# Kernel tuning notes

Measured on AMD Instinct MI355X. Metric: run time of the kernel, lower is better.

## Reference

```python
import jax, jax.numpy as jnp
import numpy as np


def setup_inputs() -> dict:
    key = jax.random.key(0)
    ks = jax.random.split(key, 5)
    b, f, h, w, c = 2, 16, 64, 64, 256
    heads, D = 8, 32
    hD = heads * D
    x = jax.random.normal(ks[0], (b, f, h, w, c), dtype=jnp.float32)
    s = 1.0 / np.sqrt(c)
    Wq = jax.random.normal(ks[1], (c, hD), dtype=jnp.float32) * s
    Wk = jax.random.normal(ks[2], (c, hD), dtype=jnp.float32) * s
    Wv = jax.random.normal(ks[3], (c, hD), dtype=jnp.float32) * s
    Wo = jax.random.normal(ks[4], (hD, c), dtype=jnp.float32) * s
    return {"x": x, "Wq": Wq, "Wk": Wk, "Wv": Wv, "Wo": Wo, "heads": heads}


def reference(x, Wq, Wk, Wv, Wo, heads):
    b, f, h, w, c = x.shape
    hD = Wq.shape[1]
    D = hD // heads
    n = h * w
    # fuse batch & frames; 1x1 conv == channel matmul
    xf = x.reshape(b * f, n, c)  # [(bf), n, c]

    def proj(W):
        # [(bf), n, hD] -> [(bf), heads, D, n]
        p = jnp.einsum('bnc,cd->bnd', xf, W)
        return p.reshape(b * f, n, heads, D).transpose(0, 2, 3, 1)

    q = jax.nn.softmax(proj(Wq), axis=-2)  # softmax over D (note: scale is dead code in source)
    k = jax.nn.softmax(proj(Wk), axis=-1)  # softmax over spatial n
    v = proj(Wv)
    context = jnp.einsum('bhdn,bhen->bhde', k, v)      # [(bf), heads, D, D]
    out = jnp.einsum('bhde,bhdn->bhen', context, q)    # [(bf), heads, D, n]
    out = out.transpose(0, 3, 1, 2).reshape(b * f, n, hD)
    out = jnp.einsum('bnd,dc->bnc', out, Wo)
    return out.reshape(b, f, h, w, c)
```

## Files before the change

### kernel.cpp

```cpp
#include <hip/hip_runtime.h>
#include <hip/hip_bf16.h>


typedef __attribute__((ext_vector_type(8))) short bf16x8;
typedef __attribute__((ext_vector_type(4))) float f32x4;

__device__ __forceinline__ unsigned short f2bf(float x) {
  __hip_bfloat16 h = __float2bfloat16(x);
  union { __hip_bfloat16 b; unsigned short u; } c; c.b = h; return c.u;
}

__device__ __forceinline__ void bar_lds() {
  asm volatile("s_waitcnt lgkmcnt(0)" ::: "memory");
  __builtin_amdgcn_s_barrier();
}

__global__ __launch_bounds__(256) void k0_prep(const float* __restrict__ Wq,
                                               const float* __restrict__ Wk,
                                               const float* __restrict__ Wv,
                                               unsigned short* __restrict__ WqT,
                                               unsigned short* __restrict__ WkvT) {
  int r = blockIdx.x, c = threadIdx.x;
  if (r < 256)      WqT [(r      )*256 + c] = f2bf(Wq[c*256 + r]);
  else if (r < 512) WkvT[(r - 256)*256 + c] = f2bf(Wk[c*256 + (r-256)]);
  else              WkvT[(r - 256)*256 + c] = f2bf(Wv[c*256 + (r-512)]);
}

__global__ __launch_bounds__(1024, 4) void k1w(const float* __restrict__ x,
                                               const unsigned short* __restrict__ WkvT,
                                               float* __restrict__ ctxp) {
  __shared__ unsigned short As[2][32*256];
  __shared__ unsigned short slab[2][512*40];
  int bid = blockIdx.x;
  size_t rowbase = (size_t)bid * 512;
  int tid = threadIdx.x;
  int lane = tid & 63, w = tid >> 6;
  int cl = lane & 15, rq = (lane >> 4) << 2, fs = lane >> 4;
  int h = w & 7;
  bool isV = w >= 8;

  bf16x8 bfr[2][8];
#pragma unroll
  for (int ni = 0; ni < 2; ++ni)
#pragma unroll
    for (int kk = 0; kk < 8; ++kk)
      bfr[ni][kk] = *(const bf16x8*)(WkvT + (size_t)(w*32 + ni*16 + cl)*256 + kk*32 + fs*8);
#pragma unroll
  for (int ni = 0; ni < 2; ++ni)
#pragma unroll
    for (int kk = 0; kk < 8; ++kk)
      asm volatile("" : "+v"(bfr[ni][kk]));

  f32x4 c2[2] = {};
  float dena0 = 0.f, dena1 = 0.f;

  int ar = tid >> 5, as_ = tid & 31;
  int aw = ar*256 + ((as_ ^ (ar & 7)) << 3);
  const float* ap = x + (rowbase + ar)*256 + as_*8;

  int ca0 = h*32 + cl, ca1 = h*32 + 16 + cl;
  int cb  = 256 + h*32 + (isV ? 16 : 0) + cl;
  int ra0 = ca0*40 + fs*8;
  int ra1 = ca1*40 + fs*8;
  int rb  = cb*40  + fs*8;

  f32x4 acc[2][2];

  auto stageA = [&](int buf, float4 v0, float4 v1) {
    unsigned short* Ab = &As[buf][0];
    union { ushort4 u4[2]; int4 i4; } pk;
    pk.u4[0].x = f2bf(v0.x); pk.u4[0].y = f2bf(v0.y); pk.u4[0].z = f2bf(v0.z); pk.u4[0].w = f2bf(v0.w);
    pk.u4[1].x = f2bf(v1.x); pk.u4[1].y = f2bf(v1.y); pk.u4[1].z = f2bf(v1.z); pk.u4[1].w = f2bf(v1.w);
    *(int4*)(&Ab[aw]) = pk.i4;
  };
  auto mainMFMA = [&](int buf) {
    unsigned short* Ab = &As[buf][0];
#pragma unroll
    for (int m = 0; m < 2; ++m)
#pragma unroll
      for (int ni = 0; ni < 2; ++ni) acc[m][ni] = (f32x4){};
#pragma unroll
    for (int kk = 0; kk < 8; ++kk) {
      int so = (((kk*4 + fs) ^ (cl & 7)) << 3);
      bf16x8 a0 = *(const bf16x8*)(&Ab[cl*256 + so]);
      bf16x8 a1 = *(const bf16x8*)(&Ab[(16 + cl)*256 + so]);
#pragma unroll
      for (int ni = 0; ni < 2; ++ni) {
        acc[0][ni] = __builtin_amdgcn_mfma_f32_16x16x32_bf16(a0, bfr[ni][kk], acc[0][ni], 0, 0, 0);
        acc[1][ni] = __builtin_amdgcn_mfma_f32_16x16x32_bf16(a1, bfr[ni][kk], acc[1][ni], 0, 0, 0);
      }
    }
  };
  auto slabWrite = [&](int buf) {
    unsigned short* sb = &slab[buf][0];
#pragma unroll
    for (int ni = 0; ni < 2; ++ni) {
      int c = w*32 + ni*16 + cl;
#pragma unroll
      for (int m = 0; m < 2; ++m) {
        int n4 = m*16 + rq;
        ushort4 wv;
        if (!isV) {
          float e0 = __expf(acc[m][ni][0]), e1 = __expf(acc[m][ni][1]);
          float e2 = __expf(acc[m][ni][2]), e3 = __expf(acc[m][ni][3]);
          if (ni == 0) dena0 += (e0 + e1) + (e2 + e3); else dena1 += (e0 + e1) + (e2 + e3);
          wv.x = f2bf(e0); wv.y = f2bf(e1); wv.z = f2bf(e2); wv.w = f2bf(e3);
        } else {
          wv.x = f2bf(acc[m][ni][0]); wv.y = f2bf(acc[m][ni][1]);
          wv.z = f2bf(acc[m][ni][2]); wv.w = f2bf(acc[m][ni][3]);
        }
        *(ushort4*)(&sb[c*40 + n4]) = wv;
      }
    }
  };
  auto ctxMFMA = [&](int buf) {
    unsigned short* sb = &slab[buf][0];
    bf16x8 af0 = *(const bf16x8*)(&sb[ra0]);
    bf16x8 af1 = *(const bf16x8*)(&sb[ra1]);
    bf16x8 bv  = *(const bf16x8*)(&sb[rb]);
    c2[0] = __builtin_amdgcn_mfma_f32_16x16x32_bf16(af0, bv, c2[0], 0, 0, 0);
    c2[1] = __builtin_amdgcn_mfma_f32_16x16x32_bf16(af1, bv, c2[1], 0, 0, 0);
  };

  float4 pa0 = *(const float4*)ap;
  float4 pa1 = *(const float4*)(ap + 4);
  stageA(0, pa0, pa1);
  {
    const float* apn = ap + 32*256;
    pa0 = *(const float4*)apn;
    pa1 = *(const float4*)(apn + 4);
  }
  bar_lds();
  mainMFMA(0);

  for (int t = 0; t < 15; ++t) {
    slabWrite(t & 1);
    stageA((t + 1) & 1, pa0, pa1);
    bar_lds();
    if (t < 14) {
      const float* apn = ap + (size_t)(t + 2)*32*256;
      pa0 = *(const float4*)apn;
      pa1 = *(const float4*)(apn + 4);
    }
    ctxMFMA(t & 1);
    mainMFMA((t + 1) & 1);
  }
  slabWrite(1);
  bar_lds();
  ctxMFMA(1);

  float* cp = ctxp + ((size_t)bid*8 + h)*1056;
  int ec = isV ? 16 + cl : cl;
#pragma unroll
  for (int di = 0; di < 2; ++di)
#pragma unroll
    for (int r = 0; r < 4; ++r)
      cp[(di*16 + rq + r)*33 + ec] = c2[di][r];
  if (!isV) {
    dena0 += __shfl_xor(dena0, 16); dena0 += __shfl_xor(dena0, 32);
    dena1 += __shfl_xor(dena1, 16); dena1 += __shfl_xor(dena1, 32);
    if (fs == 0) {
      cp[cl*33 + 32]        = dena0;
      cp[(16 + cl)*33 + 32] = dena1;
    }
  }
}

__global__ __launch_bounds__(256) void k2b_w2(const float* __restrict__ ctxp,
                                              const float* __restrict__ Wo,
                                              unsigned short* __restrict__ W2t) {
  __shared__ float clds[32*33];
  int bid = blockIdx.x;
  int h = bid & 7, bfi = bid >> 3;
  int tid = threadIdx.x;
  for (int i = tid; i < 1056; i += 256) {
    float s = 0.f;
#pragma unroll
    for (int p = 0; p < 8; ++p)
      s += ctxp[((size_t)(bfi*8 + p)*8 + h)*1056 + i];
    clds[i] = s;
  }
  __syncthreads();
  float acc[32] = {};
#pragma unroll 4
  for (int e = 0; e < 32; ++e) {
    float w = Wo[(size_t)(h*32 + e)*256 + tid];
#pragma unroll
    for (int d = 0; d < 32; ++d) acc[d] += clds[d*33 + e] * w;
  }
  unsigned short* o = W2t + ((size_t)bfi*256 + tid)*256 + h*32;
#pragma unroll
  for (int d = 0; d < 32; ++d) o[d] = f2bf(acc[d] / clds[d*33 + 32]);
}

__global__ __launch_bounds__(512, 2) void k3s(const float* __restrict__ x,
                                              const unsigned short* __restrict__ WqT,
                                              const unsigned short* __restrict__ W2t,
                                              float* __restrict__ out) {
  __shared__ unsigned short As[2][32*256];
  __shared__ unsigned short Qs[2][32*256];
  int bid = blockIdx.x;
  size_t rowbase = (size_t)bid * 256;
  int bfi = bid >> 4;
  int tid = threadIdx.x;
  int lane = tid & 63, wid = tid >> 6;
  int cl = lane & 15, rq = (lane >> 4) << 2, fs = lane >> 4;

  bf16x8 bq[2][8], bw[2][8];
#pragma unroll
  for (int nf = 0; nf < 2; ++nf)
#pragma unroll
    for (int kk = 0; kk < 8; ++kk) {
      bq[nf][kk] = *(const bf16x8*)(WqT + (size_t)(wid*32 + nf*16 + cl)*256 + kk*32 + fs*8);
      bw[nf][kk] = *(const bf16x8*)(W2t + ((size_t)bfi*256 + wid*32 + nf*16 + cl)*256 + kk*32 + fs*8);
    }

  int ar = tid >> 5, as_ = tid & 31;
  int aw0 = ar*256 + ((as_ ^ (ar & 7)) << 3);
  int aw1 = (16 + ar)*256 + ((as_ ^ (ar & 7)) << 3);
  const float* ap = x + (rowbase + ar)*256 + as_*8;

  int qslotbase = wid*4 + (rq >> 3);
  ushort4 qpk[2][2];

  auto stageA = [&](int buf, float4 v0, float4 v1, float4 v2, float4 v3) {
    unsigned short* Ab = &As[buf][0];
    union { ushort4 u4[2]; int4 i4; } pk;
    pk.u4[0].x = f2bf(v0.x); pk.u4[0].y = f2bf(v0.y); pk.u4[0].z = f2bf(v0.z); pk.u4[0].w = f2bf(v0.w);
    pk.u4[1].x = f2bf(v1.x); pk.u4[1].y = f2bf(v1.y); pk.u4[1].z = f2bf(v1.z); pk.u4[1].w = f2bf(v1.w);
    *(int4*)(&Ab[aw0]) = pk.i4;
    pk.u4[0].x = f2bf(v2.x); pk.u4[0].y = f2bf(v2.y); pk.u4[0].z = f2bf(v2.z); pk.u4[0].w = f2bf(v2.w);
    pk.u4[1].x = f2bf(v3.x); pk.u4[1].y = f2bf(v3.y); pk.u4[1].z = f2bf(v3.z); pk.u4[1].w = f2bf(v3.w);
    *(int4*)(&Ab[aw1]) = pk.i4;
  };
  auto p1soft = [&](int buf) {
    unsigned short* Ab = &As[buf][0];
    f32x4 ql[2][2] = {};
#pragma unroll
    for (int kk = 0; kk < 8; ++kk) {
      int so = (((kk*4 + fs) ^ (cl & 7)) << 3);
      bf16x8 a0 = *(const bf16x8*)(&Ab[cl*256 + so]);
      bf16x8 a1 = *(const bf16x8*)(&Ab[(16 + cl)*256 + so]);
#pragma unroll
      for (int nf = 0; nf < 2; ++nf) {
        ql[0][nf] = __builtin_amdgcn_mfma_f32_16x16x32_bf16(bq[nf][kk], a0, ql[0][nf], 0, 0, 0);
        ql[1][nf] = __builtin_amdgcn_mfma_f32_16x16x32_bf16(bq[nf][kk], a1, ql[1][nf], 0, 0, 0);
      }
    }
#pragma unroll
    for (int m = 0; m < 2; ++m) {
      float e0[4], e1[4]; float s8 = 0.f;
#pragma unroll
      for (int r = 0; r < 4; ++r) { e0[r] = __expf(ql[m][0][r]); e1[r] = __expf(ql[m][1][r]); s8 += e0[r] + e1[r]; }
      float s = s8; s += __shfl_xor(s, 16); s += __shfl_xor(s, 32);
      float inv = 1.0f / s;
      qpk[m][0].x = f2bf(e0[0]*inv); qpk[m][0].y = f2bf(e0[1]*inv); qpk[m][0].z = f2bf(e0[2]*inv); qpk[m][0].w = f2bf(e0[3]*inv);
      qpk[m][1].x = f2bf(e1[0]*inv); qpk[m][1].y = f2bf(e1[1]*inv); qpk[m][1].z = f2bf(e1[2]*inv); qpk[m][1].w = f2bf(e1[3]*inv);
    }
  };
  auto qwrite = [&](int buf) {
    unsigned short* Qb = &Qs[buf][0];
#pragma unroll
    for (int m = 0; m < 2; ++m) {
      int row = m*16 + cl;
#pragma unroll
      for (int nf = 0; nf < 2; ++nf) {
        int slot = qslotbase + nf*2;
        *(ushort4*)(&Qb[row*256 + ((slot ^ (row & 7)) << 3) + (rq & 4)]) = qpk[m][nf];
      }
    }
  };

  float4 pa0 = *(const float4*)ap;
  float4 pa1 = *(const float4*)(ap + 4);
  float4 pa2 = *(const float4*)(ap + 16*256);
  float4 pa3 = *(const float4*)(ap + 16*256 + 4);
  stageA(0, pa0, pa1, pa2, pa3);
  {
    const float* apn = ap + 32*256;
    pa0 = *(const float4*)apn;
    pa1 = *(const float4*)(apn + 4);
    pa2 = *(const float4*)(apn + 16*256);
    pa3 = *(const float4*)(apn + 16*256 + 4);
  }
  bar_lds();
  p1soft(0);

  for (int t = 0; t < 7; ++t) {
    stageA((t + 1) & 1, pa0, pa1, pa2, pa3);
    qwrite(t & 1);
    bar_lds();
    if (t < 6) {
      const float* apn = ap + (size_t)(t + 2)*32*256;
      pa0 = *(const float4*)apn;
      pa1 = *(const float4*)(apn + 4);
      pa2 = *(const float4*)(apn + 16*256);
      pa3 = *(const float4*)(apn + 16*256 + 4);
    }
    f32x4 oa[2][2] = {};
    {
      unsigned short* Qb = &Qs[t & 1][0];
#pragma unroll
      for (int kk = 0; kk < 8; ++kk) {
        int so = (((kk*4 + fs) ^ (cl & 7)) << 3);
        bf16x8 q0 = *(const bf16x8*)(&Qb[cl*256 + so]);
        bf16x8 q1 = *(const bf16x8*)(&Qb[(16 + cl)*256 + so]);
#pragma unroll
        for (int nf = 0; nf < 2; ++nf) {
          oa[0][nf] = __builtin_amdgcn_mfma_f32_16x16x32_bf16(bw[nf][kk], q0, oa[0][nf], 0, 0, 0);
          oa[1][nf] = __builtin_amdgcn_mfma_f32_16x16x32_bf16(bw[nf][kk], q1, oa[1][nf], 0, 0, 0);
        }
      }
    }
    p1soft((t + 1) & 1);
#pragma unroll
    for (int m = 0; m < 2; ++m)
#pragma unroll
      for (int nf = 0; nf < 2; ++nf)
        *(f32x4*)(&out[(rowbase + (size_t)t*32 + m*16 + cl)*256 + wid*32 + nf*16 + rq]) = oa[m][nf];
  }
  qwrite(1);
  bar_lds();
  {
    unsigned short* Qb = &Qs[1][0];
    f32x4 oa[2][2] = {};
#pragma unroll
    for (int kk = 0; kk < 8; ++kk) {
      int so = (((kk*4 + fs) ^ (cl & 7)) << 3);
      bf16x8 q0 = *(const bf16x8*)(&Qb[cl*256 + so]);
      bf16x8 q1 = *(const bf16x8*)(&Qb[(16 + cl)*256 + so]);
#pragma unroll
      for (int nf = 0; nf < 2; ++nf) {
        oa[0][nf] = __builtin_amdgcn_mfma_f32_16x16x32_bf16(bw[nf][kk], q0, oa[0][nf], 0, 0, 0);
        oa[1][nf] = __builtin_amdgcn_mfma_f32_16x16x32_bf16(bw[nf][kk], q1, oa[1][nf], 0, 0, 0);
      }
    }
#pragma unroll
    for (int m = 0; m < 2; ++m)
#pragma unroll
      for (int nf = 0; nf < 2; ++nf)
        *(f32x4*)(&out[(rowbase + (size_t)7*32 + m*16 + cl)*256 + wid*32 + nf*16 + rq]) = oa[m][nf];
  }
}

extern "C" void kernel_launch(void* const* d_in, const int* in_sizes, int n_in,
                              void* d_out, int out_size, void* d_ws, size_t ws_size,
                              hipStream_t stream) {
  const float* x  = (const float*)d_in[0];
  const float* Wq = (const float*)d_in[1];
  const float* Wk = (const float*)d_in[2];
  const float* Wv = (const float*)d_in[3];
  const float* Wo = (const float*)d_in[4];
  float* out = (float*)d_out;

  unsigned short* WkvT = (unsigned short*)d_ws;
  unsigned short* WqT  = WkvT + 131072;
  unsigned short* W2t  = WqT  + 65536;
  float*          ctxp = (float*)(W2t + 2097152);

  k0_prep <<<768,  256,  0, stream>>>(Wq, Wk, Wv, WqT, WkvT);
  k1w     <<<256,  1024, 0, stream>>>(x, WkvT, ctxp);
  k2b_w2  <<<256,  256,  0, stream>>>(ctxp, Wo, W2t);
  k3s     <<<512,  512,  0, stream>>>(x, WqT, W2t, out);
}
```

Before: 131.5 us.

## Compute Q softmax in the K/V pass and stream bf16 Q to the output kernel

The Q projection and its softmax over D move from the final kernel into the first pass over x, which already stages x tiles in LDS. Each wave runs extra MFMAs against WqT and combines partial sums with a neighbouring wave through a small LDS buffer. The normalized Q is written to a global bf16 workspace. The last kernel then reads that bf16 Q instead of re-reading fp32 x and redoing the projection. This removes a second fp32 read of x and duplicate projection work. In exchange it adds a bf16 Q round trip through memory, more register pressure in the 1024-thread kernel (the register pinning asm is dropped), and per-kk global loads of WqT inside the main loop.

After: 277.6 us. +111.2%, slower.

```diff
diff --git a/kernel.cpp b/kernel.cpp
--- a/kernel.cpp
+++ b/kernel.cpp
@@ -26,11 +26,14 @@
   else              WkvT[(r - 256)*256 + c] = f2bf(Wv[c*256 + (r-512)]);
 }
 
-__global__ __launch_bounds__(1024, 4) void k1w(const float* __restrict__ x,
+__global__ __launch_bounds__(1024, 4) void k1q(const float* __restrict__ x,
                                                const unsigned short* __restrict__ WkvT,
-                                               float* __restrict__ ctxp) {
+                                               const unsigned short* __restrict__ WqT,
+                                               float* __restrict__ ctxp,
+                                               unsigned short* __restrict__ Qs) {
   __shared__ unsigned short As[2][32*256];
   __shared__ unsigned short slab[2][512*40];
+  __shared__ float qsum[2][512];
   int bid = blockIdx.x;
   size_t rowbase = (size_t)bid * 512;
   int tid = threadIdx.x;
@@ -45,11 +48,8 @@
 #pragma unroll
     for (int kk = 0; kk < 8; ++kk)
       bfr[ni][kk] = *(const bf16x8*)(WkvT + (size_t)(w*32 + ni*16 + cl)*256 + kk*32 + fs*8);
-#pragma unroll
-  for (int ni = 0; ni < 2; ++ni)
-#pragma unroll
-    for (int kk = 0; kk < 8; ++kk)
-      asm volatile("" : "+v"(bfr[ni][kk]));
+
+  const unsigned short* bqp = WqT + (size_t)(w*16 + cl)*256 + fs*8;
 
   f32x4 c2[2] = {};
   float dena0 = 0.f, dena1 = 0.f;
@@ -64,7 +64,13 @@
   int ra1 = ca1*40 + fs*8;
   int rb  = cb*40  + fs*8;
 
+  unsigned short* qsg0 = Qs + (rowbase + cl)*256 + w*16 + rq;
+  unsigned short* qsg1 = qsg0 + 16*256;
+
   f32x4 acc[2][2];
+  f32x4 ql0, ql1;
+  float e00, e01, e02, e03, e10, e11, e12, e13;
+  float sp0, sp1;
 
   auto stageA = [&](int buf, float4 v0, float4 v1) {
     unsigned short* Ab = &As[buf][0];
@@ -79,6 +85,7 @@
     for (int m = 0; m < 2; ++m)
 #pragma unroll
       for (int ni = 0; ni < 2; ++ni) acc[m][ni] = (f32x4){};
+    ql0 = (f32x4){}; ql1 = (f32x4){};
 #pragma unroll
     for (int kk = 0; kk < 8; ++kk) {
       int so = (((kk*4 + fs) ^ (cl & 7)) << 3);
@@ -89,6 +96,9 @@
         acc[0][ni] = __builtin_amdgcn_mfma_f32_16x16x32_bf16(a0, bfr[ni][kk], acc[0][ni], 0, 0, 0);
         acc[1][ni] = __builtin_amdgcn_mfma_f32_16x16x32_bf16(a1, bfr[ni][kk], acc[1][ni], 0, 0, 0);
       }
+      bf16x8 bqk = *(const bf16x8*)(bqp + kk*32);
+      ql0 = __builtin_amdgcn_mfma_f32_16x16x32_bf16(bqk, a0, ql0, 0, 0, 0);
+      ql1 = __builtin_amdgcn_mfma_f32_16x16x32_bf16(bqk, a1, ql1, 0, 0, 0);
     }
   };
   auto slabWrite = [&](int buf) {
@@ -101,10 +111,10 @@
         int n4 = m*16 + rq;
         ushort4 wv;
         if (!isV) {
-          float e0 = __expf(acc[m][ni][0]), e1 = __expf(acc[m][ni][1]);
-          float e2 = __expf(acc[m][ni][2]), e3 = __expf(acc[m][ni][3]);
-          if (ni == 0) dena0 += (e0 + e1) + (e2 + e3); else dena1 += (e0 + e1) + (e2 + e3);
-          wv.x = f2bf(e0); wv.y = f2bf(e1); wv.z = f2bf(e2); wv.w = f2bf(e3);
+          float x0 = __expf(acc[m][ni][0]), x1 = __expf(acc[m][ni][1]);
+          float x2 = __expf(acc[m][ni][2]), x3 = __expf(acc[m][ni][3]);
+          if (ni == 0) dena0 += (x0 + x1) + (x2 + x3); else dena1 += (x0 + x1) + (x2 + x3);
+          wv.x = f2bf(x0); wv.y = f2bf(x1); wv.z = f2bf(x2); wv.w = f2bf(x3);
         } else {
           wv.x = f2bf(acc[m][ni][0]); wv.y = f2bf(acc[m][ni][1]);
           wv.z = f2bf(acc[m][ni][2]); wv.w = f2bf(acc[m][ni][3]);
@@ -112,6 +122,28 @@
         *(ushort4*)(&sb[c*40 + n4]) = wv;
       }
     }
+  };
+  auto qExp = [&](int buf) {
+    e00 = __expf(ql0[0]); e01 = __expf(ql0[1]); e02 = __expf(ql0[2]); e03 = __expf(ql0[3]);
+    e10 = __expf(ql1[0]); e11 = __expf(ql1[1]); e12 = __expf(ql1[2]); e13 = __expf(ql1[3]);
+    sp0 = (e00 + e01) + (e02 + e03);
+    sp1 = (e10 + e11) + (e12 + e13);
+    sp0 += __shfl_xor(sp0, 16); sp0 += __shfl_xor(sp0, 32);
+    sp1 += __shfl_xor(sp1, 16); sp1 += __shfl_xor(sp1, 32);
+    if (fs == 0) {
+      qsum[buf][w*32 + cl]      = sp0;
+      qsum[buf][w*32 + 16 + cl] = sp1;
+    }
+  };
+  auto qFinish = [&](int buf, int t) {
+    float t0 = sp0 + qsum[buf][(w ^ 1)*32 + cl];
+    float t1 = sp1 + qsum[buf][(w ^ 1)*32 + 16 + cl];
+    float i0 = 1.0f / t0, i1 = 1.0f / t1;
+    ushort4 u0, u1;
+    u0.x = f2bf(e00*i0); u0.y = f2bf(e01*i0); u0.z = f2bf(e02*i0); u0.w = f2bf(e03*i0);
+    u1.x = f2bf(e10*i1); u1.y = f2bf(e11*i1); u1.z = f2bf(e12*i1); u1.w = f2bf(e13*i1);
+    *(ushort4*)(qsg0 + (size_t)t*8192) = u0;
+    *(ushort4*)(qsg1 + (size_t)t*8192) = u1;
   };
   auto ctxMFMA = [&](int buf) {
     unsigned short* sb = &slab[buf][0];
@@ -135,8 +167,10 @@
 
   for (int t = 0; t < 15; ++t) {
     slabWrite(t & 1);
+    qExp(t & 1);
     stageA((t + 1) & 1, pa0, pa1);
     bar_lds();
+    qFinish(t & 1, t);
     if (t < 14) {
       const float* apn = ap + (size_t)(t + 2)*32*256;
       pa0 = *(const float4*)apn;
@@ -146,7 +180,9 @@
     mainMFMA((t + 1) & 1);
   }
   slabWrite(1);
+  qExp(1);
   bar_lds();
+  qFinish(1, 15);
   ctxMFMA(1);
 
   float* cp = ctxp + ((size_t)bid*8 + h)*1056;
@@ -193,12 +229,10 @@
   for (int d = 0; d < 32; ++d) o[d] = f2bf(acc[d] / clds[d*33 + 32]);
 }
 
-__global__ __launch_bounds__(512, 2) void k3s(const float* __restrict__ x,
-                                              const unsigned short* __restrict__ WqT,
+__global__ __launch_bounds__(512, 2) void k3b(const unsigned short* __restrict__ Qs,
                                               const unsigned short* __restrict__ W2t,
                                               float* __restrict__ out) {
   __shared__ unsigned short As[2][32*256];
-  __shared__ unsigned short Qs[2][32*256];
   int bid = blockIdx.x;
   size_t rowbase = (size_t)bid * 256;
   int bfi = bid >> 4;
@@ -206,105 +240,37 @@
   int lane = tid & 63, wid = tid >> 6;
   int cl = lane & 15, rq = (lane >> 4) << 2, fs = lane >> 4;
 
-  bf16x8 bq[2][8], bw[2][8];
+  bf16x8 bw[2][8];
 #pragma unroll
   for (int nf = 0; nf < 2; ++nf)
 #pragma unroll
-    for (int kk = 0; kk < 8; ++kk) {
-      bq[nf][kk] = *(const bf16x8*)(WqT + (size_t)(wid*32 + nf*16 + cl)*256 + kk*32 + fs*8);
+    for (int kk = 0; kk < 8; ++kk)
       bw[nf][kk] = *(const bf16x8*)(W2t + ((size_t)bfi*256 + wid*32 + nf*16 + cl)*256 + kk*32 + fs*8);
-    }
-
-  int ar = tid >> 5, as_ = tid & 31;
-  int aw0 = ar*256 + ((as_ ^ (ar & 7)) << 3);
-  int aw1 = (16 + ar)*256 + ((as_ ^ (ar & 7)) << 3);
-  const float* ap = x + (rowbase + ar)*256 + as_*8;
-
-  int qslotbase = wid*4 + (rq >> 3);
-  ushort4 qpk[2][2];
-
-  auto stageA = [&](int buf, float4 v0, float4 v1, float4 v2, float4 v3) {
-    unsigned short* Ab = &As[buf][0];
-    union { ushort4 u4[2]; int4 i4; } pk;
-    pk.u4[0].x = f2bf(v0.x); pk.u4[0].y = f2bf(v0.y); pk.u4[0].z = f2bf(v0.z); pk.u4[0].w = f2bf(v0.w);
-    pk.u4[1].x = f2bf(v1.x); pk.u4[1].y = f2bf(v1.y); pk.u4[1].z = f2bf(v1.z); pk.u4[1].w = f2bf(v1.w);
-    *(int4*)(&Ab[aw0]) = pk.i4;
-    pk.u4[0].x = f2bf(v2.x); pk.u4[0].y = f2bf(v2.y); pk.u4[0].z = f2bf(v2.z); pk.u4[0].w = f2bf(v2.w);
-    pk.u4[1].x = f2bf(v3.x); pk.u4[1].y = f2bf(v3.y); pk.u4[1].z = f2bf(v3.z); pk.u4[1].w = f2bf(v3.w);
-    *(int4*)(&Ab[aw1]) = pk.i4;
-  };
-  auto p1soft = [&](int buf) {
-    unsigned short* Ab = &As[buf][0];
-    f32x4 ql[2][2] = {};
-#pragma unroll
-    for (int kk = 0; kk < 8; ++kk) {
-      int so = (((kk*4 + fs) ^ (cl & 7)) << 3);
-      bf16x8 a0 = *(const bf16x8*)(&Ab[cl*256 + so]);
-      bf16x8 a1 = *(const bf16x8*)(&Ab[(16 + cl)*256 + so]);
-#pragma unroll
-      for (int nf = 0; nf < 2; ++nf) {
-        ql[0][nf] = __builtin_amdgcn_mfma_f32_16x16x32_bf16(bq[nf][kk], a0, ql[0][nf], 0, 0, 0);
-        ql[1][nf] = __builtin_amdgcn_mfma_f32_16x16x32_bf16(bq[nf][kk], a1, ql[1][nf], 0, 0, 0);
-      }
-    }
-#pragma unroll
-    for (int m = 0; m < 2; ++m) {
-      float e0[4], e1[4]; float s8 = 0.f;
-#pragma unroll
-      for (int r = 0; r < 4; ++r) { e0[r] = __expf(ql[m][0][r]); e1[r] = __expf(ql[m][1][r]); s8 += e0[r] + e1[r]; }
-      float s = s8; s += __shfl_xor(s, 16); s += __shfl_xor(s, 32);
-      float inv = 1.0f / s;
-      qpk[m][0].x = f2bf(e0[0]*inv); qpk[m][0].y = f2bf(e0[1]*inv); qpk[m][0].z = f2bf(e0[2]*inv); qpk[m][0].w = f2bf(e0[3]*inv);
-      qpk[m][1].x = f2bf(e1[0]*inv); qpk[m][1].y = f2bf(e1[1]*inv); qpk[m][1].z = f2bf(e1[2]*inv); qpk[m][1].w = f2bf(e1[3]*inv);
-    }
-  };
-  auto qwrite = [&](int buf) {
-    unsigned short* Qb = &Qs[buf][0];
-#pragma unroll
-    for (int m = 0; m < 2; ++m) {
-      int row = m*16 + cl;
-#pragma unroll
-      for (int nf = 0; nf < 2; ++nf) {
-        int slot = qslotbase + nf*2;
-        *(ushort4*)(&Qb[row*256 + ((slot ^ (row & 7)) << 3) + (rq & 4)]) = qpk[m][nf];
-      }
-    }
-  };
-
-  float4 pa0 = *(const float4*)ap;
-  float4 pa1 = *(const float4*)(ap + 4);
-  float4 pa2 = *(const float4*)(ap + 16*256);
-  float4 pa3 = *(const float4*)(ap + 16*256 + 4);
-  stageA(0, pa0, pa1, pa2, pa3);
-  {
-    const float* apn = ap + 32*256;
-    pa0 = *(const float4*)apn;
-    pa1 = *(const float4*)(apn + 4);
-    pa2 = *(const float4*)(apn + 16*256);
-    pa3 = *(const float4*)(apn + 16*256 + 4);
-  }
+
+  int sr = tid >> 5, ss = tid & 31;
+  const unsigned short* xsrc = Qs + (rowbase + sr)*256 + ss*8;
+  int aw0 = sr*256 + ((ss ^ (sr & 7)) << 3);
+  int aw1 = aw0 + 16*256;
+
+  int4 qa, qb;
+
+  qa = *(const int4*)xsrc;
+  qb = *(const int4*)(xsrc + 16*256);
+  *(int4*)(&As[0][aw0]) = qa;
+  *(int4*)(&As[0][aw1]) = qb;
+  qa = *(const int4*)(xsrc + 8192);
+  qb = *(const int4*)(xsrc + 8192 + 16*256);
   bar_lds();
-  p1soft(0);
-
-  for (int t = 0; t < 7; ++t) {
-    stageA((t + 1) & 1, pa0, pa1, pa2, pa3);
-    qwrite(t & 1);
-    bar_lds();
-    if (t < 6) {
-      const float* apn = ap + (size_t)(t + 2)*32*256;
-      pa0 = *(const float4*)apn;
-      pa1 = *(const float4*)(apn + 4);
-      pa2 = *(const float4*)(apn + 16*256);
-      pa3 = *(const float4*)(apn + 16*256 + 4);
-    }
+
+  for (int t = 0; t < 8; ++t) {
     f32x4 oa[2][2] = {};
     {
-      unsigned short* Qb = &Qs[t & 1][0];
+      unsigned short* Ab = &As[t & 1][0];
 #pragma unroll
       for (int kk = 0; kk < 8; ++kk) {
         int so = (((kk*4 + fs) ^ (cl & 7)) << 3);
-        bf16x8 q0 = *(const bf16x8*)(&Qb[cl*256 + so]);
-        bf16x8 q1 = *(const bf16x8*)(&Qb[(16 + cl)*256 + so]);
+        bf16x8 q0 = *(const bf16x8*)(&Ab[cl*256 + so]);
+        bf16x8 q1 = *(const bf16x8*)(&Ab[(16 + cl)*256 + so]);
 #pragma unroll
         for (int nf = 0; nf < 2; ++nf) {
           oa[0][nf] = __builtin_amdgcn_mfma_f32_16x16x32_bf16(bw[nf][kk], q0, oa[0][nf], 0, 0, 0);
@@ -312,34 +278,20 @@
         }
       }
     }
-    p1soft((t + 1) & 1);
+    if (t < 7) {
+      *(int4*)(&As[(t + 1) & 1][aw0]) = qa;
+      *(int4*)(&As[(t + 1) & 1][aw1]) = qb;
+      if (t < 6) {
+        qa = *(const int4*)(xsrc + (size_t)(t + 2)*8192);
+        qb = *(const int4*)(xsrc + (size_t)(t + 2)*8192 + 16*256);
+      }
+      bar_lds();
+    }
 #pragma unroll
     for (int m = 0; m < 2; ++m)
 #pragma unroll
       for (int nf = 0; nf < 2; ++nf)
         *(f32x4*)(&out[(rowbase + (size_t)t*32 + m*16 + cl)*256 + wid*32 + nf*16 + rq]) = oa[m][nf];
-  }
-  qwrite(1);
-  bar_lds();
-  {
-    unsigned short* Qb = &Qs[1][0];
-    f32x4 oa[2][2] = {};
-#pragma unroll
-    for (int kk = 0; kk < 8; ++kk) {
-      int so = (((kk*4 + fs) ^ (cl & 7)) << 3);
-      bf16x8 q0 = *(const bf16x8*)(&Qb[cl*256 + so]);
-      bf16x8 q1 = *(const bf16x8*)(&Qb[(16 + cl)*256 + so]);
-#pragma unroll
-      for (int nf = 0; nf < 2; ++nf) {
-        oa[0][nf] = __builtin_amdgcn_mfma_f32_16x16x32_bf16(bw[nf][kk], q0, oa[0][nf], 0, 0, 0);
-        oa[1][nf] = __builtin_amdgcn_mfma_f32_16x16x32_bf16(bw[nf][kk], q1, oa[1][nf], 0, 0, 0);
-      }
-    }
-#pragma unroll
-    for (int m = 0; m < 2; ++m)
-#pragma unroll
-      for (int nf = 0; nf < 2; ++nf)
-        *(f32x4*)(&out[(rowbase + (size_t)7*32 + m*16 + cl)*256 + wid*32 + nf*16 + rq]) = oa[m][nf];
   }
 }
 
@@ -357,9 +309,10 @@
   unsigned short* WqT  = WkvT + 131072;
   unsigned short* W2t  = WqT  + 65536;
   float*          ctxp = (float*)(W2t + 2097152);
+  unsigned short* Qs   = (unsigned short*)(ctxp + (size_t)256*8*1056);
 
   k0_prep <<<768,  256,  0, stream>>>(Wq, Wk, Wv, WqT, WkvT);
-  k1w     <<<256,  1024, 0, stream>>>(x, WkvT, ctxp);
+  k1q     <<<256,  1024, 0, stream>>>(x, WkvT, WqT, ctxp, Qs);
   k2b_w2  <<<256,  256,  0, stream>>>(ctxp, Wo, W2t);
-  k3s     <<<512,  512,  0, stream>>>(x, WqT, W2t, out);
-}
+  k3b     <<<512,  512,  0, stream>>>(Qs, W2t, out);
+}
```
